# Kernel optimization log

Measured on AMD Instinct MI355X. Metric: run time of the kernel, lower is better.

Reference implementation:

```python
import jax, jax.numpy as jnp
import numpy as np

N, E = 20000, 320000
IN_C, HID, OUT_C, HEADS = 512, 32, 40, 8
NEG_SLOPE = 0.2


def setup_inputs() -> dict:
    key = jax.random.key(0)
    ks = jax.random.split(key, 10)
    x = jax.random.normal(ks[0], (N, IN_C), dtype=jnp.float32)
    edge_index = jax.random.randint(ks[1], (2, E), 0, N, dtype=jnp.int64)
    s1 = 1.0 / np.sqrt(IN_C)
    s2 = 1.0 / np.sqrt(HEADS * HID)
    return {
        "x": x,
        "edge_index": edge_index,
        "w1": jax.random.normal(ks[2], (IN_C, HEADS * HID), dtype=jnp.float32) * s1,
        "att_src1": jax.random.normal(ks[3], (HEADS, HID), dtype=jnp.float32) * s2,
        "att_dst1": jax.random.normal(ks[4], (HEADS, HID), dtype=jnp.float32) * s2,
        "b1": jnp.zeros((HEADS * HID,), dtype=jnp.float32),
        "w2": jax.random.normal(ks[5], (HEADS * HID, OUT_C), dtype=jnp.float32) * s2,
        "att_src2": jax.random.normal(ks[6], (1, OUT_C), dtype=jnp.float32) * 0.15,
        "att_dst2": jax.random.normal(ks[7], (1, OUT_C), dtype=jnp.float32) * 0.15,
        "b2": jnp.zeros((OUT_C,), dtype=jnp.float32),
    }


def gat_conv(x, src, dst, w, att_src, att_dst, bias, heads, out_c, concat):
    n = x.shape[0]
    h = (x @ w).reshape(n, heads, out_c)            # [N,H,C]
    a_s = jnp.sum(h * att_src, axis=-1)             # [N,H]
    a_d = jnp.sum(h * att_dst, axis=-1)             # [N,H]
    e = jax.nn.leaky_relu(a_s[src] + a_d[dst], NEG_SLOPE)  # [E,H]
    # segment softmax over destination nodes (self-loops guarantee nonempty)
    m = jax.ops.segment_max(e, dst, num_segments=n)
    e = jnp.exp(e - m[dst])
    z = jax.ops.segment_sum(e, dst, num_segments=n)
    alpha = e / (z[dst] + 1e-16)                    # [E,H]
    msg = alpha[:, :, None] * h[src]                # [E,H,C]
    out = jax.ops.segment_sum(msg, dst, num_segments=n)  # [N,H,C]
    out = out.reshape(n, heads * out_c) if concat else out.mean(axis=1)
    return out + bias


def reference(x, edge_index, w1, att_src1, att_dst1, b1, w2, att_src2, att_dst2, b2):
    n = x.shape[0]
    loops = jnp.arange(n, dtype=edge_index.dtype)
    src = jnp.concatenate([edge_index[0], loops])
    dst = jnp.concatenate([edge_index[1], loops])
    h = gat_conv(x, src, dst, w1, att_src1, att_dst1, b1, HEADS, HID, True)
    h = jax.nn.elu(h)
    out = gat_conv(h, src, dst, w2, att_src2, att_dst2, b2, 1, OUT_C, False)
    return jax.nn.log_softmax(out, axis=1)
```

## Files before the change

kernel.cpp:

```cpp
#include <hip/hip_runtime.h>
#include <hip/hip_bf16.h>
#include <math.h>

#define N_NODES 20000
#define N_EDGES 320000
#define ET (N_EDGES + N_NODES)
#define IN_C 512
#define HEADS 8
#define HID 32
#define HH (HEADS * HID)
#define OUT_C 40
#define NEG_SLOPE 0.2f

typedef __attribute__((ext_vector_type(8))) short short8;
typedef __attribute__((ext_vector_type(4))) float floatx4;

static __device__ __forceinline__ unsigned short f2bf(float f) {
  __hip_bfloat16 h = __float2bfloat16(f);
  return *(unsigned short*)&h;
}
static __device__ __forceinline__ float bf2f_lo(unsigned int u) {
  return __uint_as_float(u << 16);
}
static __device__ __forceinline__ float bf2f_hi(unsigned int u) {
  return __uint_as_float(u & 0xFFFF0000u);
}

#define WCONV_BLOCKS (IN_C * HH / 256)
#define W2CONV_BLOCKS (HH * OUT_C / 256)
#define COUNT_BLOCKS ((ET + 255) / 256)
__global__ __launch_bounds__(256) void prep_kernel(
    const float* __restrict__ w1, const float* __restrict__ w2,
    const int* __restrict__ ei, unsigned short* __restrict__ wbT,
    unsigned short* __restrict__ w2bT, int* __restrict__ deg) {
  if (blockIdx.x < WCONV_BLOCKS) {
    int j = blockIdx.x * 256 + threadIdx.x;
    int k = j >> 8, n = j & 255;
    wbT[(size_t)n * IN_C + k] = f2bf(w1[j]);
  } else if (blockIdx.x < WCONV_BLOCKS + W2CONV_BLOCKS) {
    int j = (blockIdx.x - WCONV_BLOCKS) * 256 + threadIdx.x;
    int k = j / OUT_C, oc = j % OUT_C;
    w2bT[oc * HH + k] = f2bf(w2[j]);
  } else {
    int e = (blockIdx.x - WCONV_BLOCKS - W2CONV_BLOCKS) * 256 + threadIdx.x;
    if (e < ET) {
      int dst = (e < N_EDGES) ? ei[N_EDGES + e] : (e - N_EDGES);
      atomicAdd(&deg[dst], 1);
    }
  }
}

#define BM 64
#define BN 128
#define BK 32
#define APAD 40
#define GY ((N_NODES + BM - 1) / BM)
#define GEMM_BLOCKS (2 * GY)
__global__ __launch_bounds__(256) void gemm1_kernel(
    const float* __restrict__ X, const unsigned short* __restrict__ BT,
    const float* __restrict__ bias, unsigned short* __restrict__ C,
    const int* __restrict__ deg, int* __restrict__ offs, int* __restrict__ cursor) {
  if (blockIdx.x >= GEMM_BLOCKS) {
    __shared__ int wsum[4];
    int t = threadIdx.x;
    int4 buf[20];
    int s = 0;
    if (t < 250) {
      const int4* dp = (const int4*)deg + t * 20;
#pragma unroll
      for (int i = 0; i < 20; i++) {
        buf[i] = dp[i];
        s += buf[i].x + buf[i].y + buf[i].z + buf[i].w;
      }
    }
    int lane = t & 63, w = t >> 6;
    int inc = s;
    for (int o = 1; o < 64; o <<= 1) {
      int u = __shfl_up(inc, o, 64);
      if (lane >= o) inc += u;
    }
    if (lane == 63) wsum[w] = inc;
    __syncthreads();
    int waveOff = 0;
    for (int i = 0; i < w; i++) waveOff += wsum[i];
    int running = waveOff + inc - s;
    if (t < 250) {
      int base = t * 80;
#pragma unroll
      for (int i = 0; i < 20; i++) {
        int4 v = buf[i];
        int4 o;
        o.x = running;
        o.y = o.x + v.x;
        o.z = o.y + v.y;
        o.w = o.z + v.z;
        running = o.w + v.w;
        *(int4*)(offs + base + i * 4) = o;
        *(int4*)(cursor + base + i * 4) = o;
      }
    }
    if (t == 0) offs[N_NODES] = ET;
    return;
  }
  __shared__ unsigned short As[BM][APAD];
  __shared__ unsigned short Bs[BN][APAD];
  const int tid = threadIdx.x;
  const int lane = tid & 63, wave = tid >> 6;
  const int wm = (wave & 1) * 32;
  const int wn = (wave >> 1) * 64;
  const int r16 = lane & 15, q = lane >> 4;
  const int bx = blockIdx.x & 1, by = blockIdx.x >> 1;
  const int rowBase = by * BM;
  const int colBase = bx * BN;
  floatx4 acc[2][4] = {};

  for (int k0 = 0; k0 < IN_C; k0 += BK) {
    {
      int row = tid >> 2, kc = (tid & 3) * 8;
      int arow = rowBase + row;
      float4 v0 = make_float4(0.f, 0.f, 0.f, 0.f), v1 = v0;
      if (arow < N_NODES) {
        const float* p = X + (size_t)arow * IN_C + k0 + kc;
        v0 = *(const float4*)p;
        v1 = *(const float4*)(p + 4);
      }
      unsigned short tmp[8] = {f2bf(v0.x), f2bf(v0.y), f2bf(v0.z), f2bf(v0.w),
                               f2bf(v1.x), f2bf(v1.y), f2bf(v1.z), f2bf(v1.w)};
      *(float4*)&As[row][kc] = *(const float4*)tmp;
    }
#pragma unroll
    for (int i = 0; i < 2; i++) {
      int c = tid + i * 256;
      int row = c >> 2, kc = (c & 3) * 8;
      float4 v = *(const float4*)(BT + (size_t)(colBase + row) * IN_C + k0 + kc);
      *(float4*)&Bs[row][kc] = v;
    }
    __syncthreads();
    short8 afrag[2], bfrag[4];
#pragma unroll
    for (int mt = 0; mt < 2; mt++)
      afrag[mt] = *(const short8*)&As[wm + mt * 16 + r16][q * 8];
#pragma unroll
    for (int nt = 0; nt < 4; nt++)
      bfrag[nt] = *(const short8*)&Bs[wn + nt * 16 + r16][q * 8];
#pragma unroll
    for (int mt = 0; mt < 2; mt++)
#pragma unroll
      for (int nt = 0; nt < 4; nt++)
        acc[mt][nt] = __builtin_amdgcn_mfma_f32_16x16x32_bf16(
            afrag[mt], bfrag[nt], acc[mt][nt], 0, 0, 0);
    __syncthreads();
  }
#pragma unroll
  for (int mt = 0; mt < 2; mt++) {
#pragma unroll
    for (int nt = 0; nt < 4; nt++) {
      int col = colBase + wn + nt * 16 + r16;
      float bb = bias[col];
#pragma unroll
      for (int r = 0; r < 4; r++) {
        int row = rowBase + wm + mt * 16 + q * 4 + r;
        if (row < N_NODES) C[(size_t)row * HH + col] = f2bf(acc[mt][nt][r] + bb);
      }
    }
  }
}

#define FILL_BLOCKS ((ET + 255) / 256)
#define ATTN1_BLOCKS (N_NODES / 4)
__global__ __launch_bounds__(256) void fill_attn1_kernel(
    const int* __restrict__ ei, int* __restrict__ cursor, int* __restrict__ csr,
    const unsigned short* __restrict__ h1b, const float* __restrict__ asrc,
    const float* __restrict__ adst, float* __restrict__ as1, float* __restrict__ ad1) {
  if (blockIdx.x < FILL_BLOCKS) {
    int e = blockIdx.x * 256 + threadIdx.x;
    if (e >= ET) return;
    int src, dst;
    if (e < N_EDGES) { src = ei[e]; dst = ei[N_EDGES + e]; }
    else { src = e - N_EDGES; dst = src; }
    int pos = atomicAdd(&cursor[dst], 1);
    csr[pos] = src;
  } else {
    int wave = threadIdx.x >> 6, lane = threadIdx.x & 63;
    int n = (blockIdx.x - FILL_BLOCKS) * 4 + wave;
    int c4 = lane * 4;
    uint2 raw = *(const uint2*)(h1b + (size_t)n * HH + c4);
    float h0 = bf2f_lo(raw.x), h1 = bf2f_hi(raw.x);
    float h2 = bf2f_lo(raw.y), h3 = bf2f_hi(raw.y);
    float4 sa = *(const float4*)(asrc + c4);
    float4 sd = *(const float4*)(adst + c4);
    float ps = h0 * sa.x + h1 * sa.y + h2 * sa.z + h3 * sa.w;
    float pd = h0 * sd.x + h1 * sd.y + h2 * sd.z + h3 * sd.w;
#pragma unroll
    for (int o = 4; o > 0; o >>= 1) {
      ps += __shfl_down(ps, o, 8);
      pd += __shfl_down(pd, o, 8);
    }
    if ((lane & 7) == 0) {
      as1[n * HEADS + (lane >> 3)] = ps;
      ad1[n * HEADS + (lane >> 3)] = pd;
    }
  }
}

#define NPB 16
#define H2ROW 264
__global__ __launch_bounds__(512, 8) void layer1_fused_kernel(
    const unsigned short* __restrict__ h1b, const float* __restrict__ as1,
    const float* __restrict__ ad1, const int* __restrict__ offs,
    const int* __restrict__ csr, const float* __restrict__ b1,
    const unsigned short* __restrict__ w2bT, const float* __restrict__ b2,
    const float* __restrict__ asrc2, const float* __restrict__ adst2,
    float* __restrict__ h3, float* __restrict__ as2, float* __restrict__ ad2) {
  __shared__ __align__(16) unsigned short h2s[NPB][H2ROW];
  __shared__ float psum[3][NPB], pdsum[3][NPB];
  const int tid = threadIdx.x;
  const int wave = tid >> 6, lane = tid & 63;
  const int r16 = lane & 15, q = lane >> 4;
  const int nodeBase = blockIdx.x * NPB;

  const int strm = lane >> 5;
  const int l32 = lane & 31;
  const int c8 = l32 * 8;
  const int head = l32 >> 2;
  float4 bb = *(const float4*)(b1 + c8 + strm * 4);
#pragma unroll
  for (int i = 0; i < 2; i++) {
    int local = wave * 2 + i;
    int n = nodeBase + local;
    int beg = offs[n], end = offs[n + 1];
    int cnt = end - beg;
    float ad = ad1[n * HEADS + head];
    float acc[8] = {};
    float l = 0.f;
    for (int kb = 0; kb < cnt; kb += 64) {
      int nb = (cnt - kb < 64) ? (cnt - kb) : 64;
      int myidx = (lane < nb) ? csr[beg + kb + lane] : 0;
      int j = strm;
      if (j < nb) {
        int src = __shfl(myidx, j, 64);
        uint4 r = *(const uint4*)(h1b + ((unsigned)src << 8) + c8);
        float e = as1[src * HEADS + head];
        for (j += 2; j < nb; j += 2) {
          int src2 = __shfl(myidx, j, 64);
          uint4 r2 = *(const uint4*)(h1b + ((unsigned)src2 << 8) + c8);
          float e2 = as1[src2 * HEADS + head];
          float tt = e + ad;
          tt = (tt > 0.f) ? tt : NEG_SLOPE * tt;
          float p = __expf(tt);
          l += p;
          acc[0] = fmaf(p, bf2f_lo(r.x), acc[0]);
          acc[1] = fmaf(p, bf2f_hi(r.x), acc[1]);
          acc[2] = fmaf(p, bf2f_lo(r.y), acc[2]);
          acc[3] = fmaf(p, bf2f_hi(r.y), acc[3]);
          acc[4] = fmaf(p, bf2f_lo(r.z), acc[4]);
          acc[5] = fmaf(p, bf2f_hi(r.z), acc[5]);
          acc[6] = fmaf(p, bf2f_lo(r.w), acc[6]);
          acc[7] = fmaf(p, bf2f_hi(r.w), acc[7]);
          r = r2; e = e2;
        }
        float tt = e + ad;
        tt = (tt > 0.f) ? tt : NEG_SLOPE * tt;
        float p = __expf(tt);
        l += p;
        acc[0] = fmaf(p, bf2f_lo(r.x), acc[0]);
        acc[1] = fmaf(p, bf2f_hi(r.x), acc[1]);
        acc[2] = fmaf(p, bf2f_lo(r.y), acc[2]);
        acc[3] = fmaf(p, bf2f_hi(r.y), acc[3]);
        acc[4] = fmaf(p, bf2f_lo(r.z), acc[4]);
        acc[5] = fmaf(p, bf2f_hi(r.z), acc[5]);
        acc[6] = fmaf(p, bf2f_lo(r.w), acc[6]);
        acc[7] = fmaf(p, bf2f_hi(r.w), acc[7]);
      }
    }
#pragma unroll
    for (int j = 0; j < 8; j++) acc[j] += __shfl_xor(acc[j], 32, 64);
    l += __shfl_xor(l, 32, 64);
    float li = 1.f / (l + 1e-16f);
    float v0 = (strm ? acc[4] : acc[0]) * li + bb.x;
    float v1 = (strm ? acc[5] : acc[1]) * li + bb.y;
    float v2 = (strm ? acc[6] : acc[2]) * li + bb.z;
    float v3 = (strm ? acc[7] : acc[3]) * li + bb.w;
    v0 = (v0 > 0.f) ? v0 : __expf(v0) - 1.f;
    v1 = (v1 > 0.f) ? v1 : __expf(v1) - 1.f;
    v2 = (v2 > 0.f) ? v2 : __expf(v2) - 1.f;
    v3 = (v3 > 0.f) ? v3 : __expf(v3) - 1.f;
    uint2 w;
    w.x = (unsigned)f2bf(v0) | ((unsigned)f2bf(v1) << 16);
    w.y = (unsigned)f2bf(v2) | ((unsigned)f2bf(v3) << 16);
    *(uint2*)&h2s[local][c8 + strm * 4] = w;
  }
  __syncthreads();

  if (wave < 3) {
    int col = wave * 16 + r16;
    int colc = (col < OUT_C) ? col : 0;
    short8 bfrag[8];
#pragma unroll
    for (int s = 0; s < 8; s++)
      bfrag[s] = *(const short8*)(w2bT + colc * HH + s * 32 + q * 8);
    float sa = 0.f, sd = 0.f, b2c = 0.f;
    if (col < OUT_C) { sa = asrc2[col]; sd = adst2[col]; b2c = b2[col]; }
    floatx4 dacc = {};
#pragma unroll
    for (int s = 0; s < 8; s++) {
      short8 afrag = *(const short8*)&h2s[r16][s * 32 + q * 8];
      dacc = __builtin_amdgcn_mfma_f32_16x16x32_bf16(afrag, bfrag[s], dacc, 0, 0, 0);
    }
    float psr[4], pdr[4];
#pragma unroll
    for (int r = 0; r < 4; r++) {
      float val = dacc[r] + b2c;
      if (col < OUT_C)
        h3[(size_t)(nodeBase + q * 4 + r) * OUT_C + col] = val;
      psr[r] = val * sa;
      pdr[r] = val * sd;
    }
#pragma unroll
    for (int o = 8; o > 0; o >>= 1) {
#pragma unroll
      for (int r = 0; r < 4; r++) {
        psr[r] += __shfl_down(psr[r], o, 16);
        pdr[r] += __shfl_down(pdr[r], o, 16);
      }
    }
    if (r16 == 0) {
#pragma unroll
      for (int r = 0; r < 4; r++) {
        psum[wave][q * 4 + r] = psr[r];
        pdsum[wave][q * 4 + r] = pdr[r];
      }
    }
  }
  __syncthreads();
  if (tid < NPB) {
    as2[nodeBase + tid] = psum[0][tid] + psum[1][tid] + psum[2][tid];
    ad2[nodeBase + tid] = pdsum[0][tid] + pdsum[1][tid] + pdsum[2][tid];
  }
}

__global__ __launch_bounds__(256) void agg2_kernel(
    const float* __restrict__ h3, const float* __restrict__ as2,
    const float* __restrict__ ad2, const int* __restrict__ offs,
    const int* __restrict__ csr, const float* __restrict__ b2,
    float* __restrict__ out) {
  int n = blockIdx.x * 4 + (threadIdx.x >> 6);
  int t = threadIdx.x & 63;
  bool act = (t < OUT_C);
  int beg = offs[n], end = offs[n + 1];
  float ad = ad2[n];
  float l0 = 0.f, l1 = 0.f, l2 = 0.f, l3 = 0.f;
  float a0 = 0.f, a1 = 0.f, a2 = 0.f, a3 = 0.f;
  int k = beg;
  for (; k + 3 < end; k += 4) {
    int s0 = csr[k], s1 = csr[k + 1], s2 = csr[k + 2], s3 = csr[k + 3];
    float e0 = as2[s0] + ad, e1 = as2[s1] + ad;
    float e2 = as2[s2] + ad, e3 = as2[s3] + ad;
    e0 = (e0 > 0.f) ? e0 : NEG_SLOPE * e0;
    e1 = (e1 > 0.f) ? e1 : NEG_SLOPE * e1;
    e2 = (e2 > 0.f) ? e2 : NEG_SLOPE * e2;
    e3 = (e3 > 0.f) ? e3 : NEG_SLOPE * e3;
    float p0 = __expf(e0), p1 = __expf(e1), p2 = __expf(e2), p3 = __expf(e3);
    l0 += p0; l1 += p1; l2 += p2; l3 += p3;
    float h0 = act ? h3[(size_t)s0 * OUT_C + t] : 0.f;
    float h1 = act ? h3[(size_t)s1 * OUT_C + t] : 0.f;
    float h2 = act ? h3[(size_t)s2 * OUT_C + t] : 0.f;
    float h3v = act ? h3[(size_t)s3 * OUT_C + t] : 0.f;
    a0 = fmaf(p0, h0, a0);
    a1 = fmaf(p1, h1, a1);
    a2 = fmaf(p2, h2, a2);
    a3 = fmaf(p3, h3v, a3);
  }
  for (; k < end; k++) {
    int s0 = csr[k];
    float e0 = as2[s0] + ad;
    e0 = (e0 > 0.f) ? e0 : NEG_SLOPE * e0;
    float p0 = __expf(e0);
    l0 += p0;
    float h0 = act ? h3[(size_t)s0 * OUT_C + t] : 0.f;
    a0 = fmaf(p0, h0, a0);
  }
  float l = (l0 + l1) + (l2 + l3), acc = (a0 + a1) + (a2 + a3);
  float v = acc / (l + 1e-16f) + (act ? b2[t] : 0.f);
  float x = act ? v : -INFINITY;
  float mx = x;
  for (int o = 32; o > 0; o >>= 1) mx = fmaxf(mx, __shfl_down(mx, o, 64));
  mx = __shfl(mx, 0, 64);
  float ex = act ? __expf(v - mx) : 0.f;
  float s = ex;
  for (int o = 32; o > 0; o >>= 1) s += __shfl_down(s, o, 64);
  s = __shfl(s, 0, 64);
  if (act) out[(size_t)n * OUT_C + t] = v - mx - logf(s);
}

extern "C" void kernel_launch(void* const* d_in, const int* in_sizes, int n_in,
                              void* d_out, int out_size, void* d_ws, size_t ws_size,
                              hipStream_t stream) {
  const float* x     = (const float*)d_in[0];
  const int*   ei    = (const int*)d_in[1];
  const float* w1    = (const float*)d_in[2];
  const float* asrc1 = (const float*)d_in[3];
  const float* adst1 = (const float*)d_in[4];
  const float* b1    = (const float*)d_in[5];
  const float* w2    = (const float*)d_in[6];
  const float* asrc2 = (const float*)d_in[7];
  const float* adst2 = (const float*)d_in[8];
  const float* b2    = (const float*)d_in[9];
  float* out = (float*)d_out;

  float* fw = (float*)d_ws;
  float* as1   = fw;  fw += (size_t)N_NODES * HEADS;
  float* ad1   = fw;  fw += (size_t)N_NODES * HEADS;
  float* h3    = fw;  fw += (size_t)N_NODES * OUT_C;
  float* as2   = fw;  fw += N_NODES;
  float* ad2   = fw;  fw += N_NODES;
  unsigned short* h1b  = (unsigned short*)fw;  fw += (size_t)N_NODES * HH / 2;
  unsigned short* wbT  = (unsigned short*)fw;  fw += (size_t)IN_C * HH / 2;
  unsigned short* w2bT = (unsigned short*)fw;  fw += (size_t)HH * OUT_C / 2;
  int* deg    = (int*)fw;
  int* offs   = deg + N_NODES;
  int* cursor = offs + N_NODES + 4;
  int* csr    = cursor + N_NODES;

  hipMemsetAsync(deg, 0, N_NODES * sizeof(int), stream);

  prep_kernel<<<WCONV_BLOCKS + W2CONV_BLOCKS + COUNT_BLOCKS, 256, 0, stream>>>(
      w1, w2, ei, wbT, w2bT, deg);
  gemm1_kernel<<<GEMM_BLOCKS + 1, 256, 0, stream>>>(x, wbT, b1, h1b, deg, offs, cursor);
  fill_attn1_kernel<<<FILL_BLOCKS + ATTN1_BLOCKS, 256, 0, stream>>>(
      ei, cursor, csr, h1b, asrc1, adst1, as1, ad1);
  layer1_fused_kernel<<<N_NODES / NPB, 512, 0, stream>>>(
      h1b, as1, ad1, offs, csr, b1, w2bT, b2, asrc2, adst2, h3, as2, ad2);
  agg2_kernel<<<N_NODES / 4, 256, 0, stream>>>(h3, as2, ad2, offs, csr, b2, out);
}
```

Measured before the change: 208.9 us.

## Fuse layer-1 attention scores into GEMM epilogue and batch agg2 edge loads

Computes the per-head source and destination attention logits directly in the GEMM epilogue from fp32 accumulators, removing the separate attn1 pass that re-read the bf16 h1 matrix. The GEMM block order is remapped so groups of row tiles share both column tiles, which should improve L2 reuse of X. agg2 now loads up to 64 neighbor indices and exp weights cooperatively across the wave and broadcasts them with shuffles, rather than every lane redundantly loading csr and as2. The attention logits now come from unrounded fp32 values, a slight numeric change, and the epilogue adds shuffle reductions.

```diff
diff --git a/kernel.cpp b/kernel.cpp
--- a/kernel.cpp
+++ b/kernel.cpp
@@ -58,7 +58,9 @@
 #define GEMM_BLOCKS (2 * GY)
 __global__ __launch_bounds__(256) void gemm1_kernel(
     const float* __restrict__ X, const unsigned short* __restrict__ BT,
-    const float* __restrict__ bias, unsigned short* __restrict__ C,
+    const float* __restrict__ bias, const float* __restrict__ asrc,
+    const float* __restrict__ adst, unsigned short* __restrict__ C,
+    float* __restrict__ as1, float* __restrict__ ad1,
     const int* __restrict__ deg, int* __restrict__ offs, int* __restrict__ cursor) {
   if (blockIdx.x >= GEMM_BLOCKS) {
     __shared__ int wsum[4];
@@ -102,6 +104,18 @@
     if (t == 0) offs[N_NODES] = ET;
     return;
   }
+  int d = blockIdx.x;
+  int by, bx;
+  const int FULL = (GY / 8) * 16;
+  if (d < FULL) {
+    int c = d >> 4, j = d & 15;
+    by = c * 8 + (j & 7);
+    bx = j >> 3;
+  } else {
+    int dd = d - FULL;
+    by = (GY / 8) * 8 + (dd & 0);
+    bx = dd;
+  }
   __shared__ unsigned short As[BM][APAD];
   __shared__ unsigned short Bs[BN][APAD];
   const int tid = threadIdx.x;
@@ -109,7 +123,6 @@
   const int wm = (wave & 1) * 32;
   const int wn = (wave >> 1) * 64;
   const int r16 = lane & 15, q = lane >> 4;
-  const int bx = blockIdx.x & 1, by = blockIdx.x >> 1;
   const int rowBase = by * BM;
   const int colBase = bx * BN;
   floatx4 acc[2][4] = {};
@@ -151,56 +164,61 @@
             afrag[mt], bfrag[nt], acc[mt][nt], 0, 0, 0);
     __syncthreads();
   }
+  float sa[4], sd[4], bbv[4];
+#pragma unroll
+  for (int nt = 0; nt < 4; nt++) {
+    int col = colBase + wn + nt * 16 + r16;
+    sa[nt] = asrc[col];
+    sd[nt] = adst[col];
+    bbv[nt] = bias[col];
+  }
+  const int headBase = (colBase + wn) >> 5;
 #pragma unroll
   for (int mt = 0; mt < 2; mt++) {
 #pragma unroll
     for (int nt = 0; nt < 4; nt++) {
       int col = colBase + wn + nt * 16 + r16;
-      float bb = bias[col];
 #pragma unroll
       for (int r = 0; r < 4; r++) {
         int row = rowBase + wm + mt * 16 + q * 4 + r;
-        if (row < N_NODES) C[(size_t)row * HH + col] = f2bf(acc[mt][nt][r] + bb);
+        if (row < N_NODES) C[(size_t)row * HH + col] = f2bf(acc[mt][nt][r] + bbv[nt]);
+      }
+    }
+#pragma unroll
+    for (int h = 0; h < 2; h++) {
+#pragma unroll
+      for (int r = 0; r < 4; r++) {
+        float v0 = acc[mt][2 * h][r] + bbv[2 * h];
+        float v1 = acc[mt][2 * h + 1][r] + bbv[2 * h + 1];
+        float ps = v0 * sa[2 * h] + v1 * sa[2 * h + 1];
+        float pd = v0 * sd[2 * h] + v1 * sd[2 * h + 1];
+#pragma unroll
+        for (int o = 1; o < 16; o <<= 1) {
+          ps += __shfl_xor(ps, o, 64);
+          pd += __shfl_xor(pd, o, 64);
+        }
+        if (r16 == 0) {
+          int row = rowBase + wm + mt * 16 + q * 4 + r;
+          if (row < N_NODES) {
+            as1[row * HEADS + headBase + h] = ps;
+            ad1[row * HEADS + headBase + h] = pd;
+          }
+        }
       }
     }
   }
 }
 
 #define FILL_BLOCKS ((ET + 255) / 256)
-#define ATTN1_BLOCKS (N_NODES / 4)
-__global__ __launch_bounds__(256) void fill_attn1_kernel(
-    const int* __restrict__ ei, int* __restrict__ cursor, int* __restrict__ csr,
-    const unsigned short* __restrict__ h1b, const float* __restrict__ asrc,
-    const float* __restrict__ adst, float* __restrict__ as1, float* __restrict__ ad1) {
-  if (blockIdx.x < FILL_BLOCKS) {
-    int e = blockIdx.x * 256 + threadIdx.x;
-    if (e >= ET) return;
-    int src, dst;
-    if (e < N_EDGES) { src = ei[e]; dst = ei[N_EDGES + e]; }
-    else { src = e - N_EDGES; dst = src; }
-    int pos = atomicAdd(&cursor[dst], 1);
-    csr[pos] = src;
-  } else {
-    int wave = threadIdx.x >> 6, lane = threadIdx.x & 63;
-    int n = (blockIdx.x - FILL_BLOCKS) * 4 + wave;
-    int c4 = lane * 4;
-    uint2 raw = *(const uint2*)(h1b + (size_t)n * HH + c4);
-    float h0 = bf2f_lo(raw.x), h1 = bf2f_hi(raw.x);
-    float h2 = bf2f_lo(raw.y), h3 = bf2f_hi(raw.y);
-    float4 sa = *(const float4*)(asrc + c4);
-    float4 sd = *(const float4*)(adst + c4);
-    float ps = h0 * sa.x + h1 * sa.y + h2 * sa.z + h3 * sa.w;
-    float pd = h0 * sd.x + h1 * sd.y + h2 * sd.z + h3 * sd.w;
-#pragma unroll
-    for (int o = 4; o > 0; o >>= 1) {
-      ps += __shfl_down(ps, o, 8);
-      pd += __shfl_down(pd, o, 8);
-    }
-    if ((lane & 7) == 0) {
-      as1[n * HEADS + (lane >> 3)] = ps;
-      ad1[n * HEADS + (lane >> 3)] = pd;
-    }
-  }
+__global__ __launch_bounds__(256) void fill_kernel(
+    const int* __restrict__ ei, int* __restrict__ cursor, int* __restrict__ csr) {
+  int e = blockIdx.x * 256 + threadIdx.x;
+  if (e >= ET) return;
+  int src, dst;
+  if (e < N_EDGES) { src = ei[e]; dst = ei[N_EDGES + e]; }
+  else { src = e - N_EDGES; dst = src; }
+  int pos = atomicAdd(&cursor[dst], 1);
+  csr[pos] = src;
 }
 
 #define NPB 16
@@ -348,39 +366,47 @@
   int t = threadIdx.x & 63;
   bool act = (t < OUT_C);
   int beg = offs[n], end = offs[n + 1];
+  int cnt = end - beg;
   float ad = ad2[n];
-  float l0 = 0.f, l1 = 0.f, l2 = 0.f, l3 = 0.f;
+  float l = 0.f;
   float a0 = 0.f, a1 = 0.f, a2 = 0.f, a3 = 0.f;
-  int k = beg;
-  for (; k + 3 < end; k += 4) {
-    int s0 = csr[k], s1 = csr[k + 1], s2 = csr[k + 2], s3 = csr[k + 3];
-    float e0 = as2[s0] + ad, e1 = as2[s1] + ad;
-    float e2 = as2[s2] + ad, e3 = as2[s3] + ad;
-    e0 = (e0 > 0.f) ? e0 : NEG_SLOPE * e0;
-    e1 = (e1 > 0.f) ? e1 : NEG_SLOPE * e1;
-    e2 = (e2 > 0.f) ? e2 : NEG_SLOPE * e2;
-    e3 = (e3 > 0.f) ? e3 : NEG_SLOPE * e3;
-    float p0 = __expf(e0), p1 = __expf(e1), p2 = __expf(e2), p3 = __expf(e3);
-    l0 += p0; l1 += p1; l2 += p2; l3 += p3;
-    float h0 = act ? h3[(size_t)s0 * OUT_C + t] : 0.f;
-    float h1 = act ? h3[(size_t)s1 * OUT_C + t] : 0.f;
-    float h2 = act ? h3[(size_t)s2 * OUT_C + t] : 0.f;
-    float h3v = act ? h3[(size_t)s3 * OUT_C + t] : 0.f;
-    a0 = fmaf(p0, h0, a0);
-    a1 = fmaf(p1, h1, a1);
-    a2 = fmaf(p2, h2, a2);
-    a3 = fmaf(p3, h3v, a3);
-  }
-  for (; k < end; k++) {
-    int s0 = csr[k];
-    float e0 = as2[s0] + ad;
-    e0 = (e0 > 0.f) ? e0 : NEG_SLOPE * e0;
-    float p0 = __expf(e0);
-    l0 += p0;
-    float h0 = act ? h3[(size_t)s0 * OUT_C + t] : 0.f;
-    a0 = fmaf(p0, h0, a0);
-  }
-  float l = (l0 + l1) + (l2 + l3), acc = (a0 + a1) + (a2 + a3);
+  for (int kb = 0; kb < cnt; kb += 64) {
+    int nb = (cnt - kb < 64) ? (cnt - kb) : 64;
+    int sj = 0;
+    float pj = 0.f;
+    if (t < nb) {
+      sj = csr[beg + kb + t];
+      float e = as2[sj] + ad;
+      e = (e > 0.f) ? e : NEG_SLOPE * e;
+      pj = __expf(e);
+    }
+    float ll = pj;
+#pragma unroll
+    for (int o = 32; o > 0; o >>= 1) ll += __shfl_xor(ll, o, 64);
+    l += ll;
+    int j = 0;
+    for (; j + 3 < nb; j += 4) {
+      int s0 = __shfl(sj, j, 64), s1 = __shfl(sj, j + 1, 64);
+      int s2 = __shfl(sj, j + 2, 64), s3 = __shfl(sj, j + 3, 64);
+      float p0 = __shfl(pj, j, 64), p1 = __shfl(pj, j + 1, 64);
+      float p2 = __shfl(pj, j + 2, 64), p3 = __shfl(pj, j + 3, 64);
+      float h0 = act ? h3[(size_t)s0 * OUT_C + t] : 0.f;
+      float h1 = act ? h3[(size_t)s1 * OUT_C + t] : 0.f;
+      float h2 = act ? h3[(size_t)s2 * OUT_C + t] : 0.f;
+      float h3v = act ? h3[(size_t)s3 * OUT_C + t] : 0.f;
+      a0 = fmaf(p0, h0, a0);
+      a1 = fmaf(p1, h1, a1);
+      a2 = fmaf(p2, h2, a2);
+      a3 = fmaf(p3, h3v, a3);
+    }
+    for (; j < nb; j++) {
+      int s0 = __shfl(sj, j, 64);
+      float p0 = __shfl(pj, j, 64);
+      float h0 = act ? h3[(size_t)s0 * OUT_C + t] : 0.f;
+      a0 = fmaf(p0, h0, a0);
+    }
+  }
+  float acc = (a0 + a1) + (a2 + a3);
   float v = acc / (l + 1e-16f) + (act ? b2[t] : 0.f);
   float x = act ? v : -INFINITY;
   float mx = x;
@@ -426,9 +452,9 @@
 
   prep_kernel<<<WCONV_BLOCKS + W2CONV_BLOCKS + COUNT_BLOCKS, 256, 0, stream>>>(
       w1, w2, ei, wbT, w2bT, deg);
-  gemm1_kernel<<<GEMM_BLOCKS + 1, 256, 0, stream>>>(x, wbT, b1, h1b, deg, offs, cursor);
-  fill_attn1_kernel<<<FILL_BLOCKS + ATTN1_BLOCKS, 256, 0, stream>>>(
-      ei, cursor, csr, h1b, asrc1, adst1, as1, ad1);
+  gemm1_kernel<<<GEMM_BLOCKS + 1, 256, 0, stream>>>(
+      x, wbT, b1, asrc1, adst1, h1b, as1, ad1, deg, offs, cursor);
+  fill_kernel<<<FILL_BLOCKS, 256, 0, stream>>>(ei, cursor, csr);
   layer1_fused_kernel<<<N_NODES / NPB, 512, 0, stream>>>(
       h1b, as1, ad1, offs, csr, b1, w2bT, b2, asrc2, adst2, h3, as2, ad2);
   agg2_kernel<<<N_NODES / 4, 256, 0, stream>>>(h3, as2, ad2, offs, csr, b2, out);
```

Result: no change. 204.9 us (-1.9%).
